# Kernel optimization log

Hardware: AMD Instinct MI355X
Metric: run time of the kernel (lower is better)

Reference implementation:

```python
import jax, jax.numpy as jnp
import numpy as np

N, B, D, K, H = 30000, 16, 32, 8, 8
DIST = 5.0
EPS = 1e-6


def setup_inputs() -> dict:
    key = jax.random.key(0)
    ks = jax.random.split(key, 16)
    sc = 1.0 / np.sqrt(D)
    inp = {
        'pos': jax.random.uniform(ks[0], (N, 3), jnp.float32) * 20.0,
        'node_features': jax.random.normal(ks[1], (N, D), jnp.float32),
        'batch': jnp.sort(jax.random.randint(ks[2], (N,), 0, B, dtype=jnp.int32)),
        'bessel_weights': jnp.linspace(jnp.pi, K * jnp.pi, K).astype(jnp.float32),
        'init_dummy': jax.random.normal(ks[3], (D,), jnp.float32),
        'Wq_dummy': jax.random.normal(ks[4], (D, D), jnp.float32) * sc,
        'Wq_graph': jax.random.normal(ks[5], (D, D), jnp.float32) * sc,
        'Wdot': jax.random.normal(ks[6], (D, D), jnp.float32) * sc,
        'W1_kd': jax.random.normal(ks[7], (K, H), jnp.float32) / np.sqrt(K),
        'W2_kd': jax.random.normal(ks[8], (H, D * D), jnp.float32) / np.sqrt(H),
        'W1_vd': jax.random.normal(ks[9], (K, H), jnp.float32) / np.sqrt(K),
        'W2_vd': jax.random.normal(ks[10], (H, D * D), jnp.float32) / np.sqrt(H),
        'W1_kg': jax.random.normal(ks[11], (K, H), jnp.float32) / np.sqrt(K),
        'W2_kg': jax.random.normal(ks[12], (H, D * D), jnp.float32) / np.sqrt(H),
        'W1_vg': jax.random.normal(ks[13], (K, H), jnp.float32) / np.sqrt(K),
        'W2_vg': jax.random.normal(ks[14], (H, D * D), jnp.float32) / np.sqrt(H),
    }
    return inp


def reference(pos, node_features, batch, bessel_weights, init_dummy,
              Wq_dummy, Wq_graph, Wdot,
              W1_kd, W2_kd, W1_vd, W2_vd, W1_kg, W2_kg, W1_vg, W2_vg):
    scale = 1.0 / np.sqrt(D)

    # --- dummy edge features: per-batch z extents + bessel basis ---
    z = pos[:, 2]                                            # [N]
    z_min = jax.ops.segment_min(z, batch, num_segments=B)    # [B]
    z_max = jax.ops.segment_max(z, batch, num_segments=B)    # [B]
    bot_len = z - z_min[batch] + DIST                        # [N]
    top_len = z_max[batch] + DIST - z                        # [N]

    def bessel(x):  # [N] -> [N,K]
        return jnp.sin(bessel_weights * x[:, None]) / (x[:, None] + EPS)

    edge = jnp.stack([bessel(bot_len), bessel(top_len)], axis=1)  # [N,2,K]

    # --- init dummy node features [B, 2, D] ---
    dummy = jnp.broadcast_to(init_dummy, (B, 2, D))

    def gen_w(W1, W2):  # conditional weight generator (silu MLP)
        return (jax.nn.silu(edge @ W1) @ W2).reshape(N, 2, D, D)

    # --- dummy nodes attend over graph nodes (segment softmax) ---
    wk = gen_w(W1_kd, W2_kd)                                 # [N,2,D,D]
    wv = gen_w(W1_vd, W2_vd)
    q = (dummy @ Wq_dummy)[batch]                            # [N,2,D]
    k = jnp.einsum('nd,nsde->nse', node_features, wk)        # [N,2,D]
    v = jnp.einsum('nd,nsde->nse', node_features, wv)
    s = jnp.einsum('nsq,qk,nsk->ns', q, Wdot, k) * scale     # [N,2]
    m = jax.ops.segment_max(s, batch, num_segments=B)
    e = jnp.exp(s - m[batch])
    zsum = jax.ops.segment_sum(e, batch, num_segments=B)
    attn = e / zsum[batch]                                   # [N,2]
    dummy_new = dummy + jax.ops.segment_sum(attn[..., None] * v, batch, num_segments=B)

    # --- graph nodes attend over (2) dummy nodes ---
    wkg = gen_w(W1_kg, W2_kg)
    wvg = gen_w(W1_vg, W2_vg)
    d_per = dummy_new[batch]                                 # [N,2,D]
    kg = jnp.einsum('nsd,nsde->nse', d_per, wkg)
    vg = jnp.einsum('nsd,nsde->nse', d_per, wvg)
    qg = node_features @ Wq_graph                            # [N,D]
    sg = jnp.einsum('nq,qk,nsk->ns', qg, Wdot, kg) * scale   # [N,2]
    ag = jax.nn.softmax(sg, axis=1)
    x_new = node_features + jnp.einsum('ns,nsd->nd', ag, vg)  # [N,D]
    return x_new
```

## Files before the change

kernel.cpp:

```cpp
#include <hip/hip_runtime.h>
#include <math.h>

#define NN 30000
#define BB 16
#define DD 32
#define KK 8
#define HH 8
#define DIST_C 5.0f
#define EPS_C 1e-6f
#define SCALE_C 0.17677669529663687f

#define WS_ZMIN 0
#define WS_ZMAX 16
#define WS_ZSUM 32
#define WS_QW   64
#define WS_PK   96
#define WS_WC   352
#define WS_T    1376
#define WS_AKG  9568
#define WS_AVG  17760

__device__ __forceinline__ unsigned fencode(float f) {
    unsigned u = __float_as_uint(f);
    return (u & 0x80000000u) ? ~u : (u | 0x80000000u);
}
__device__ __forceinline__ float fdecode(unsigned c) {
    return __uint_as_float((c & 0x80000000u) ? (c ^ 0x80000000u) : ~c);
}
__device__ __forceinline__ float silu(float x) { return x / (1.0f + expf(-x)); }

__global__ __launch_bounds__(256) void k_init(const float* __restrict__ init_dummy,
                                              const float* __restrict__ Wq_dummy,
                                              const float* __restrict__ Wdot,
                                              const float* __restrict__ W2_kd,
                                              const float* __restrict__ Wq_graph,
                                              float* __restrict__ ws) {
    __shared__ float qvec[32];
    __shared__ float qWl[32];
    int t = threadIdx.x;
    unsigned* wsu = (unsigned*)ws;
    if (t < 16) { wsu[WS_ZMIN + t] = 0xFFFFFFFFu; wsu[WS_ZMAX + t] = 0u; }
    if (t < 32) ws[WS_ZSUM + t] = 0.0f;
    for (int i = t; i < 8192; i += 256) ws[WS_T + i] = 0.0f;
    if (t < 32) {
        float acc = 0.0f;
        for (int d = 0; d < 32; ++d) acc += init_dummy[d] * Wq_dummy[d * 32 + t];
        qvec[t] = acc;
    }
    __syncthreads();
    if (t < 32) {
        float acc = 0.0f;
        for (int e = 0; e < 32; ++e) acc += qvec[e] * Wdot[e * 32 + t];
        qWl[t] = acc;
        ws[WS_QW + t] = acc;
    }
    __syncthreads();
    {
        int h = t >> 5, d = t & 31;
        float acc = 0.0f;
        for (int e = 0; e < 32; ++e) acc += W2_kd[h * 1024 + d * 32 + e] * qWl[e];
        ws[WS_PK + t] = acc;
    }
    for (int i = t; i < 1024; i += 256) {
        int d = i >> 5, e = i & 31;
        float acc = 0.0f;
        for (int m = 0; m < 32; ++m) acc += Wq_graph[d * 32 + m] * Wdot[m * 32 + e];
        ws[WS_WC + i] = acc;
    }
}

__global__ __launch_bounds__(256) void k_zminmax(const float* __restrict__ pos,
                                                 const int* __restrict__ batch,
                                                 float* __restrict__ ws) {
    __shared__ unsigned zl[16], zh[16];
    int t = threadIdx.x;
    if (t < 16) { zl[t] = 0xFFFFFFFFu; zh[t] = 0u; }
    __syncthreads();
    int n = blockIdx.x * 256 + t;
    if (n < NN) {
        unsigned c = fencode(pos[3 * n + 2]);
        int b = batch[n];
        atomicMin(&zl[b], c);
        atomicMax(&zh[b], c);
    }
    __syncthreads();
    unsigned* wsu = (unsigned*)ws;
    if (t < 16) {
        if (zl[t] != 0xFFFFFFFFu) atomicMin(&wsu[WS_ZMIN + t], zl[t]);
        if (zh[t] != 0u)          atomicMax(&wsu[WS_ZMAX + t], zh[t]);
    }
}

#define LWS 17
#define LFS 36
__global__ __launch_bounds__(256) void k_phase1(const float* __restrict__ pos,
                                                const int* __restrict__ batch,
                                                const float* __restrict__ nf,
                                                const float* __restrict__ bw,
                                                const float* __restrict__ W1_kd,
                                                const float* __restrict__ W1_vd,
                                                float* __restrict__ ws) {
    __shared__ float Lw[256 * LWS];
    __shared__ float Lf[256 * LFS];
    __shared__ int   Lb[256];
    __shared__ float W1kd[64], W1vd[64], Pk[256], zsl[32], bwl[8];
    int t = threadIdx.x;
    if (t < 64) { W1kd[t] = W1_kd[t]; W1vd[t] = W1_vd[t]; }
    Pk[t] = ws[WS_PK + t];
    if (t < 32) zsl[t] = 0.0f;
    if (t < 8) bwl[t] = bw[t];
    __syncthreads();

    int n = blockIdx.x * 256 + t;
    if (n < NN) {
        int b = batch[n];
        unsigned* wsu = (unsigned*)ws;
        float z = pos[3 * n + 2];
        float zmin = fdecode(wsu[WS_ZMIN + b]);
        float zmax = fdecode(wsu[WS_ZMAX + b]);
        float xl[2];
        xl[0] = z - zmin + DIST_C;
        xl[1] = zmax + DIST_C - z;
        float edge[2][8];
        #pragma unroll
        for (int s = 0; s < 2; ++s) {
            float inv = 1.0f / (xl[s] + EPS_C);
            #pragma unroll
            for (int k = 0; k < 8; ++k) edge[s][k] = sinf(bwl[k] * xl[s]) * inv;
        }
        float f[32];
        const float4* nf4 = (const float4*)nf;
        float4* Lf4 = (float4*)Lf;
        #pragma unroll
        for (int j = 0; j < 8; ++j) {
            float4 v = nf4[n * 8 + j];
            f[4 * j] = v.x; f[4 * j + 1] = v.y; f[4 * j + 2] = v.z; f[4 * j + 3] = v.w;
            Lf4[t * 9 + j] = v;
        }
        float u[8];
        #pragma unroll
        for (int h = 0; h < 8; ++h) {
            float acc = 0.0f;
            #pragma unroll
            for (int d = 0; d < 32; ++d) acc += f[d] * Pk[h * 32 + d];
            u[h] = acc;
        }
        float ev[2];
        #pragma unroll
        for (int s = 0; s < 2; ++s) {
            float sacc = 0.0f;
            #pragma unroll
            for (int h = 0; h < 8; ++h) {
                float pre = 0.0f;
                #pragma unroll
                for (int k = 0; k < 8; ++k) pre += edge[s][k] * W1kd[k * 8 + h];
                sacc += silu(pre) * u[h];
            }
            ev[s] = expf(sacc * SCALE_C);
            atomicAdd(&zsl[b * 2 + s], ev[s]);
        }
        #pragma unroll
        for (int s = 0; s < 2; ++s) {
            #pragma unroll
            for (int h = 0; h < 8; ++h) {
                float pre = 0.0f;
                #pragma unroll
                for (int k = 0; k < 8; ++k) pre += edge[s][k] * W1vd[k * 8 + h];
                Lw[t * LWS + s * 8 + h] = ev[s] * silu(pre);
            }
        }
        Lb[t] = b;
    } else {
        Lb[t] = -1;
    }
    __syncthreads();
    if (t < 32 && zsl[t] != 0.0f) atomicAdd(&ws[WS_ZSUM + t], zsl[t]);

    int base = blockIdx.x * 256;
    int count = NN - base; if (count > 256) count = 256;
    int bf = Lb[0], bl = Lb[count - 1];
    int wave = t >> 6, lane = t & 63;
    int sh = lane & 15;
    int dg = lane >> 4;
    int i0 = wave * 64;
    int i1 = i0 + 64; if (i1 > count) i1 = count;
    const float4* Lf4r = (const float4*)Lf;
    for (int b2 = bf; b2 <= bl; ++b2) {
        float a0 = 0.f, a1 = 0.f, a2 = 0.f, a3 = 0.f;
        float a4 = 0.f, a5 = 0.f, a6 = 0.f, a7 = 0.f;
        for (int i = i0; i < i1; ++i) {
            if (Lb[i] != b2) continue;
            float w = Lw[i * LWS + sh];
            float4 x0 = Lf4r[i * 9 + 2 * dg];
            float4 x1 = Lf4r[i * 9 + 2 * dg + 1];
            a0 += w * x0.x; a1 += w * x0.y; a2 += w * x0.z; a3 += w * x0.w;
            a4 += w * x1.x; a5 += w * x1.y; a6 += w * x1.z; a7 += w * x1.w;
        }
        float* Tb = ws + WS_T + b2 * 512 + sh * 32 + dg * 8;
        atomicAdd(&Tb[0], a0); atomicAdd(&Tb[1], a1);
        atomicAdd(&Tb[2], a2); atomicAdd(&Tb[3], a3);
        atomicAdd(&Tb[4], a4); atomicAdd(&Tb[5], a5);
        atomicAdd(&Tb[6], a6); atomicAdd(&Tb[7], a7);
    }
}

__global__ __launch_bounds__(256) void k_batch(const float* __restrict__ init_dummy,
                                               const float* __restrict__ W2_vd,
                                               const float* __restrict__ W2_kg,
                                               const float* __restrict__ W2_vg,
                                               float* __restrict__ ws) {
    int bs = blockIdx.x;
    int b = bs >> 1, s = bs & 1;
    int t = threadIdx.x;
    __shared__ float Tl[256];
    __shared__ float dn[32];
    Tl[t] = ws[WS_T + b * 512 + s * 256 + t];
    __syncthreads();
    if (t < 32) {
        float acc = 0.0f;
        #pragma unroll
        for (int h = 0; h < 8; ++h) {
            #pragma unroll
            for (int d = 0; d < 32; ++d)
                acc += Tl[h * 32 + d] * W2_vd[h * 1024 + d * 32 + t];
        }
        float zs = ws[WS_ZSUM + b * 2 + s];
        dn[t] = init_dummy[t] + acc / zs;
    }
    __syncthreads();
    {
        int h = t >> 5, e = t & 31;
        float ak = 0.0f, av = 0.0f;
        #pragma unroll
        for (int d = 0; d < 32; ++d) {
            float dv = dn[d];
            ak += dv * W2_kg[h * 1024 + d * 32 + e];
            av += dv * W2_vg[h * 1024 + d * 32 + e];
        }
        ws[WS_AKG + b * 512 + s * 256 + t] = ak;
        ws[WS_AVG + b * 512 + s * 256 + t] = av;
    }
}

__global__ __launch_bounds__(256) void k_final(const float* __restrict__ pos,
                                               const int* __restrict__ batch,
                                               const float* __restrict__ nf,
                                               const float* __restrict__ bw,
                                               const float* __restrict__ W1_kg,
                                               const float* __restrict__ W1_vg,
                                               const float* __restrict__ ws,
                                               float* __restrict__ out) {
    __shared__ float Wc[1024];
    __shared__ float W1kg[64], W1vg[64], bwl[8];
    int t = threadIdx.x;
    for (int i = t; i < 1024; i += 256) Wc[i] = ws[WS_WC + i];
    if (t < 64) { W1kg[t] = W1_kg[t]; W1vg[t] = W1_vg[t]; }
    if (t < 8) bwl[t] = bw[t];
    __syncthreads();
    int n = blockIdx.x * 256 + t;
    if (n >= NN) return;

    int b = batch[n];
    const unsigned* wsu = (const unsigned*)ws;
    float z = pos[3 * n + 2];
    float zmin = fdecode(wsu[WS_ZMIN + b]);
    float zmax = fdecode(wsu[WS_ZMAX + b]);
    float xl[2];
    xl[0] = z - zmin + DIST_C;
    xl[1] = zmax + DIST_C - z;
    float edge[2][8];
    #pragma unroll
    for (int s = 0; s < 2; ++s) {
        float inv = 1.0f / (xl[s] + EPS_C);
        #pragma unroll
        for (int k = 0; k < 8; ++k) edge[s][k] = sinf(bwl[k] * xl[s]) * inv;
    }
    float akg[2][8], avgg[2][8];
    #pragma unroll
    for (int s = 0; s < 2; ++s) {
        #pragma unroll
        for (int h = 0; h < 8; ++h) {
            float pk = 0.0f, pv = 0.0f;
            #pragma unroll
            for (int k = 0; k < 8; ++k) {
                pk += edge[s][k] * W1kg[k * 8 + h];
                pv += edge[s][k] * W1vg[k * 8 + h];
            }
            akg[s][h] = silu(pk);
            avgg[s][h] = silu(pv);
        }
    }
    float f[32];
    const float4* nf4 = (const float4*)nf;
    float4 fv4[8];
    #pragma unroll
    for (int j = 0; j < 8; ++j) {
        float4 v = nf4[n * 8 + j];
        fv4[j] = v;
        f[4 * j] = v.x; f[4 * j + 1] = v.y; f[4 * j + 2] = v.z; f[4 * j + 3] = v.w;
    }
    float4 q4[8];
    #pragma unroll
    for (int j = 0; j < 8; ++j) { q4[j].x = 0; q4[j].y = 0; q4[j].z = 0; q4[j].w = 0; }
    const float4* Wc4 = (const float4*)Wc;
    #pragma unroll
    for (int d = 0; d < 32; ++d) {
        float fd = f[d];
        #pragma unroll
        for (int j = 0; j < 8; ++j) {
            float4 w = Wc4[d * 8 + j];
            q4[j].x += fd * w.x; q4[j].y += fd * w.y; q4[j].z += fd * w.z; q4[j].w += fd * w.w;
        }
    }
    const float4* Ak4 = (const float4*)(ws + WS_AKG);
    const float4* Av4 = (const float4*)(ws + WS_AVG);
    float sg[2];
    #pragma unroll
    for (int s = 0; s < 2; ++s) {
        float acc = 0.0f;
        #pragma unroll
        for (int h = 0; h < 8; ++h) {
            int rb = b * 128 + s * 64 + h * 8;
            float dotv = 0.0f;
            #pragma unroll
            for (int j = 0; j < 8; ++j) {
                float4 a = Ak4[rb + j];
                dotv += q4[j].x * a.x + q4[j].y * a.y + q4[j].z * a.z + q4[j].w * a.w;
            }
            acc += akg[s][h] * dotv;
        }
        sg[s] = acc * SCALE_C;
    }
    float mm = fmaxf(sg[0], sg[1]);
    float e0 = expf(sg[0] - mm), e1 = expf(sg[1] - mm);
    float inv = 1.0f / (e0 + e1);
    float ag0 = e0 * inv, ag1 = e1 * inv;
    float4 x4[8];
    #pragma unroll
    for (int j = 0; j < 8; ++j) x4[j] = fv4[j];
    #pragma unroll
    for (int s = 0; s < 2; ++s) {
        float ags = (s == 0) ? ag0 : ag1;
        #pragma unroll
        for (int h = 0; h < 8; ++h) {
            float wv = ags * avgg[s][h];
            int rb = b * 128 + s * 64 + h * 8;
            #pragma unroll
            for (int j = 0; j < 8; ++j) {
                float4 a = Av4[rb + j];
                x4[j].x += wv * a.x; x4[j].y += wv * a.y; x4[j].z += wv * a.z; x4[j].w += wv * a.w;
            }
        }
    }
    float4* out4 = (float4*)out;
    #pragma unroll
    for (int j = 0; j < 8; ++j) out4[n * 8 + j] = x4[j];
}

extern "C" void kernel_launch(void* const* d_in, const int* in_sizes, int n_in,
                              void* d_out, int out_size, void* d_ws, size_t ws_size,
                              hipStream_t stream) {
    const float* pos        = (const float*)d_in[0];
    const float* nf         = (const float*)d_in[1];
    const int*   batch      = (const int*)d_in[2];
    const float* bw         = (const float*)d_in[3];
    const float* init_dummy = (const float*)d_in[4];
    const float* Wq_dummy   = (const float*)d_in[5];
    const float* Wq_graph   = (const float*)d_in[6];
    const float* Wdot       = (const float*)d_in[7];
    const float* W1_kd      = (const float*)d_in[8];
    const float* W2_kd      = (const float*)d_in[9];
    const float* W1_vd      = (const float*)d_in[10];
    const float* W2_vd      = (const float*)d_in[11];
    const float* W1_kg      = (const float*)d_in[12];
    const float* W2_kg      = (const float*)d_in[13];
    const float* W1_vg      = (const float*)d_in[14];
    const float* W2_vg      = (const float*)d_in[15];
    float* ws  = (float*)d_ws;
    float* out = (float*)d_out;

    int nblk = (NN + 255) / 256;
    hipLaunchKernelGGL(k_init, dim3(1), dim3(256), 0, stream,
                       init_dummy, Wq_dummy, Wdot, W2_kd, Wq_graph, ws);
    hipLaunchKernelGGL(k_zminmax, dim3(nblk), dim3(256), 0, stream, pos, batch, ws);
    hipLaunchKernelGGL(k_phase1, dim3(nblk), dim3(256), 0, stream,
                       pos, batch, nf, bw, W1_kd, W1_vd, ws);
    hipLaunchKernelGGL(k_batch, dim3(32), dim3(256), 0, stream,
                       init_dummy, W2_vd, W2_kg, W2_vg, ws);
    hipLaunchKernelGGL(k_final, dim3(nblk), dim3(256), 0, stream,
                       pos, batch, nf, bw, W1_kg, W1_vg, ws, out);
}
```

Baseline: 147.0 us.

## Fuse all stages into one persistent kernel with grid-wide atomic barriers

Replaces the five launches (init, z min/max, phase1, per-batch, final) with one 118-block kernel. Three spin-wait grid barriers on a workspace counter, cleared by a memset, separate the stages. Per-node data (features, edge basis, all four W1 projections, the query) stays in registers and is no longer recomputed or reloaded in the final stage. Z extents are reduced through per-block partials instead of global atomics. The cost is barrier spin overhead, more register pressure, and reliance on all blocks being co-resident, which 118 blocks on this GPU should satisfy.

```diff
diff --git a/kernel.cpp b/kernel.cpp
--- a/kernel.cpp
+++ b/kernel.cpp
@@ -3,22 +3,21 @@
 
 #define NN 30000
 #define BB 16
-#define DD 32
-#define KK 8
-#define HH 8
+#define NBLK 118
 #define DIST_C 5.0f
 #define EPS_C 1e-6f
 #define SCALE_C 0.17677669529663687f
 
-#define WS_ZMIN 0
-#define WS_ZMAX 16
-#define WS_ZSUM 32
-#define WS_QW   64
-#define WS_PK   96
-#define WS_WC   352
-#define WS_T    1376
-#define WS_AKG  9568
-#define WS_AVG  17760
+#define WS_BAR  0
+#define WS_PZM  8
+#define WS_PZX  2056
+#define WS_ZSUM 4104
+#define WS_T    4136
+#define WS_AKG  12328
+#define WS_AVG  20520
+
+#define LWS 17
+#define LFS 36
 
 __device__ __forceinline__ unsigned fencode(float f) {
     unsigned u = __float_as_uint(f);
@@ -29,95 +28,129 @@
 }
 __device__ __forceinline__ float silu(float x) { return x / (1.0f + expf(-x)); }
 
-__global__ __launch_bounds__(256) void k_init(const float* __restrict__ init_dummy,
-                                              const float* __restrict__ Wq_dummy,
-                                              const float* __restrict__ Wdot,
-                                              const float* __restrict__ W2_kd,
-                                              const float* __restrict__ Wq_graph,
-                                              float* __restrict__ ws) {
-    __shared__ float qvec[32];
-    __shared__ float qWl[32];
+__device__ __forceinline__ void gbarrier(unsigned* cnt, unsigned target) {
+    __syncthreads();
+    if (threadIdx.x == 0) {
+        __threadfence();
+        __hip_atomic_fetch_add(cnt, 1u, __ATOMIC_ACQ_REL, __HIP_MEMORY_SCOPE_AGENT);
+        while (__hip_atomic_load(cnt, __ATOMIC_ACQUIRE, __HIP_MEMORY_SCOPE_AGENT) < target) {
+            __builtin_amdgcn_s_sleep(2);
+        }
+    }
+    __syncthreads();
+}
+
+__global__ __launch_bounds__(256) void k_fused(
+    const float* __restrict__ pos, const int* __restrict__ batch,
+    const float* __restrict__ nf, const float* __restrict__ bw,
+    const float* __restrict__ init_dummy, const float* __restrict__ Wq_dummy,
+    const float* __restrict__ Wq_graph, const float* __restrict__ Wdot,
+    const float* __restrict__ W1_kd, const float* __restrict__ W2_kd,
+    const float* __restrict__ W1_vd, const float* __restrict__ W2_vd,
+    const float* __restrict__ W1_kg, const float* __restrict__ W2_kg,
+    const float* __restrict__ W1_vg, const float* __restrict__ W2_vg,
+    float* __restrict__ ws, float* __restrict__ out)
+{
+    __shared__ float Lw[256 * LWS];
+    __shared__ float Lf[256 * LFS];
+    __shared__ int   Lb[256];
+    __shared__ float W1kd[64], W1vd[64], W1kg[64], W1vg[64];
+    __shared__ float Pk[256], Wc[1024], qv[64], zsl[32], bwl[8];
+    __shared__ unsigned zl[16], zh[16];
+
     int t = threadIdx.x;
     unsigned* wsu = (unsigned*)ws;
-    if (t < 16) { wsu[WS_ZMIN + t] = 0xFFFFFFFFu; wsu[WS_ZMAX + t] = 0u; }
-    if (t < 32) ws[WS_ZSUM + t] = 0.0f;
-    for (int i = t; i < 8192; i += 256) ws[WS_T + i] = 0.0f;
+    unsigned* barc = wsu + WS_BAR;
+
+    if (t < 64) { W1kd[t] = W1_kd[t]; W1vd[t] = W1_vd[t];
+                  W1kg[t] = W1_kg[t]; W1vg[t] = W1_vg[t]; }
+    if (t < 8)  bwl[t] = bw[t];
+    if (t < 16) { zl[t] = 0u; zh[t] = 0u; }
+    if (t < 32) zsl[t] = 0.0f;
     if (t < 32) {
         float acc = 0.0f;
         for (int d = 0; d < 32; ++d) acc += init_dummy[d] * Wq_dummy[d * 32 + t];
-        qvec[t] = acc;
+        qv[t] = acc;
     }
     __syncthreads();
     if (t < 32) {
         float acc = 0.0f;
-        for (int e = 0; e < 32; ++e) acc += qvec[e] * Wdot[e * 32 + t];
-        qWl[t] = acc;
-        ws[WS_QW + t] = acc;
+        for (int e = 0; e < 32; ++e) acc += qv[e] * Wdot[e * 32 + t];
+        qv[32 + t] = acc;
+    }
+
+    int n = blockIdx.x * 256 + t;
+    bool act = n < NN;
+    float z = 0.0f; int b = 0;
+    float f[32]; float4 fv4[8];
+    #pragma unroll
+    for (int j = 0; j < 8; ++j) { fv4[j].x = fv4[j].y = fv4[j].z = fv4[j].w = 0.0f; }
+    if (act) {
+        z = pos[3 * n + 2];
+        b = batch[n];
+        const float4* nf4 = (const float4*)nf;
+        float4* Lf4 = (float4*)Lf;
+        #pragma unroll
+        for (int j = 0; j < 8; ++j) {
+            float4 v = nf4[n * 8 + j];
+            fv4[j] = v;
+            f[4*j] = v.x; f[4*j+1] = v.y; f[4*j+2] = v.z; f[4*j+3] = v.w;
+            Lf4[t * 9 + j] = v;
+        }
+        atomicMax(&zl[b], fencode(-z));
+        atomicMax(&zh[b], fencode(z));
+        Lb[t] = b;
+    } else {
+        #pragma unroll
+        for (int j = 0; j < 32; ++j) f[j] = 0.0f;
+        Lb[t] = -1;
     }
     __syncthreads();
     {
         int h = t >> 5, d = t & 31;
         float acc = 0.0f;
-        for (int e = 0; e < 32; ++e) acc += W2_kd[h * 1024 + d * 32 + e] * qWl[e];
-        ws[WS_PK + t] = acc;
+        for (int e = 0; e < 32; ++e) acc += W2_kd[h * 1024 + d * 32 + e] * qv[32 + e];
+        Pk[t] = acc;
     }
     for (int i = t; i < 1024; i += 256) {
         int d = i >> 5, e = i & 31;
         float acc = 0.0f;
         for (int m = 0; m < 32; ++m) acc += Wq_graph[d * 32 + m] * Wdot[m * 32 + e];
-        ws[WS_WC + i] = acc;
-    }
-}
-
-__global__ __launch_bounds__(256) void k_zminmax(const float* __restrict__ pos,
-                                                 const int* __restrict__ batch,
-                                                 float* __restrict__ ws) {
-    __shared__ unsigned zl[16], zh[16];
-    int t = threadIdx.x;
-    if (t < 16) { zl[t] = 0xFFFFFFFFu; zh[t] = 0u; }
-    __syncthreads();
-    int n = blockIdx.x * 256 + t;
-    if (n < NN) {
-        unsigned c = fencode(pos[3 * n + 2]);
-        int b = batch[n];
-        atomicMin(&zl[b], c);
-        atomicMax(&zh[b], c);
-    }
-    __syncthreads();
-    unsigned* wsu = (unsigned*)ws;
+        Wc[i] = acc;
+    }
     if (t < 16) {
-        if (zl[t] != 0xFFFFFFFFu) atomicMin(&wsu[WS_ZMIN + t], zl[t]);
-        if (zh[t] != 0u)          atomicMax(&wsu[WS_ZMAX + t], zh[t]);
-    }
-}
-
-#define LWS 17
-#define LFS 36
-__global__ __launch_bounds__(256) void k_phase1(const float* __restrict__ pos,
-                                                const int* __restrict__ batch,
-                                                const float* __restrict__ nf,
-                                                const float* __restrict__ bw,
-                                                const float* __restrict__ W1_kd,
-                                                const float* __restrict__ W1_vd,
-                                                float* __restrict__ ws) {
-    __shared__ float Lw[256 * LWS];
-    __shared__ float Lf[256 * LFS];
-    __shared__ int   Lb[256];
-    __shared__ float W1kd[64], W1vd[64], Pk[256], zsl[32], bwl[8];
-    int t = threadIdx.x;
-    if (t < 64) { W1kd[t] = W1_kd[t]; W1vd[t] = W1_vd[t]; }
-    Pk[t] = ws[WS_PK + t];
-    if (t < 32) zsl[t] = 0.0f;
-    if (t < 8) bwl[t] = bw[t];
-    __syncthreads();
-
-    int n = blockIdx.x * 256 + t;
-    if (n < NN) {
-        int b = batch[n];
-        unsigned* wsu = (unsigned*)ws;
-        float z = pos[3 * n + 2];
-        float zmin = fdecode(wsu[WS_ZMIN + b]);
-        float zmax = fdecode(wsu[WS_ZMAX + b]);
+        wsu[WS_PZM + t * 128 + blockIdx.x] = zl[t];
+        wsu[WS_PZX + t * 128 + blockIdx.x] = zh[t];
+        zl[t] = 0u; zh[t] = 0u;
+    }
+    {
+        int g = blockIdx.x * 256 + t;
+        if (g < 8224) ws[WS_ZSUM + g] = 0.0f;
+    }
+    gbarrier(barc, NBLK);
+
+    {
+        int b4 = t >> 4, c = t & 15;
+        unsigned m0 = 0u, m1 = 0u;
+        int i0 = c * 8, i1 = i0 + 8; if (i1 > NBLK) i1 = NBLK;
+        for (int i = i0; i < i1; ++i) {
+            unsigned p0 = wsu[WS_PZM + b4 * 128 + i];
+            unsigned p1 = wsu[WS_PZX + b4 * 128 + i];
+            m0 = m0 > p0 ? m0 : p0;
+            m1 = m1 > p1 ? m1 : p1;
+        }
+        atomicMax(&zl[b4], m0);
+        atomicMax(&zh[b4], m1);
+    }
+    __syncthreads();
+
+    float akg[2][8], avgg[2][8];
+    float4 q4[8];
+    #pragma unroll
+    for (int j = 0; j < 8; ++j) { q4[j].x = q4[j].y = q4[j].z = q4[j].w = 0.0f; }
+    {
+        float zmin = -fdecode(zl[b]);
+        float zmax =  fdecode(zh[b]);
         float xl[2];
         xl[0] = z - zmin + DIST_C;
         xl[1] = zmax + DIST_C - z;
@@ -128,15 +161,6 @@
             #pragma unroll
             for (int k = 0; k < 8; ++k) edge[s][k] = sinf(bwl[k] * xl[s]) * inv;
         }
-        float f[32];
-        const float4* nf4 = (const float4*)nf;
-        float4* Lf4 = (float4*)Lf;
-        #pragma unroll
-        for (int j = 0; j < 8; ++j) {
-            float4 v = nf4[n * 8 + j];
-            f[4 * j] = v.x; f[4 * j + 1] = v.y; f[4 * j + 2] = v.z; f[4 * j + 3] = v.w;
-            Lf4[t * 9 + j] = v;
-        }
         float u[8];
         #pragma unroll
         for (int h = 0; h < 8; ++h) {
@@ -145,216 +169,152 @@
             for (int d = 0; d < 32; ++d) acc += f[d] * Pk[h * 32 + d];
             u[h] = acc;
         }
-        float ev[2];
         #pragma unroll
         for (int s = 0; s < 2; ++s) {
             float sacc = 0.0f;
             #pragma unroll
             for (int h = 0; h < 8; ++h) {
-                float pre = 0.0f;
+                float pkd = 0.0f, pvd = 0.0f, pkg = 0.0f, pvg = 0.0f;
                 #pragma unroll
-                for (int k = 0; k < 8; ++k) pre += edge[s][k] * W1kd[k * 8 + h];
-                sacc += silu(pre) * u[h];
-            }
-            ev[s] = expf(sacc * SCALE_C);
-            atomicAdd(&zsl[b * 2 + s], ev[s]);
-        }
+                for (int k = 0; k < 8; ++k) {
+                    float e8 = edge[s][k];
+                    pkd += e8 * W1kd[k * 8 + h];
+                    pvd += e8 * W1vd[k * 8 + h];
+                    pkg += e8 * W1kg[k * 8 + h];
+                    pvg += e8 * W1vg[k * 8 + h];
+                }
+                sacc += silu(pkd) * u[h];
+                Lw[t * LWS + s * 8 + h] = silu(pvd);
+                akg[s][h] = silu(pkg);
+                avgg[s][h] = silu(pvg);
+            }
+            float ev = act ? expf(sacc * SCALE_C) : 0.0f;
+            if (act) atomicAdd(&zsl[b * 2 + s], ev);
+            #pragma unroll
+            for (int h = 0; h < 8; ++h) Lw[t * LWS + s * 8 + h] *= ev;
+        }
+        const float4* Wc4 = (const float4*)Wc;
+        #pragma unroll
+        for (int d = 0; d < 32; ++d) {
+            float fd = f[d];
+            #pragma unroll
+            for (int j = 0; j < 8; ++j) {
+                float4 w = Wc4[d * 8 + j];
+                q4[j].x += fd * w.x; q4[j].y += fd * w.y;
+                q4[j].z += fd * w.z; q4[j].w += fd * w.w;
+            }
+        }
+    }
+    __syncthreads();
+    if (t < 32 && zsl[t] != 0.0f) atomicAdd(&ws[WS_ZSUM + t], zsl[t]);
+
+    {
+        int base = blockIdx.x * 256;
+        int count = NN - base; if (count > 256) count = 256;
+        int bf = Lb[0], bl = Lb[count - 1];
+        int wave = t >> 6, lane = t & 63;
+        int sh = lane & 15;
+        int dg = lane >> 4;
+        int i0 = wave * 64;
+        int i1 = i0 + 64; if (i1 > count) i1 = count;
+        const float4* Lf4r = (const float4*)Lf;
+        for (int b2 = bf; b2 <= bl; ++b2) {
+            float a0=0.f,a1=0.f,a2=0.f,a3=0.f,a4=0.f,a5=0.f,a6=0.f,a7=0.f;
+            for (int i = i0; i < i1; ++i) {
+                if (Lb[i] != b2) continue;
+                float w = Lw[i * LWS + sh];
+                float4 x0 = Lf4r[i * 9 + 2 * dg];
+                float4 x1 = Lf4r[i * 9 + 2 * dg + 1];
+                a0 += w * x0.x; a1 += w * x0.y; a2 += w * x0.z; a3 += w * x0.w;
+                a4 += w * x1.x; a5 += w * x1.y; a6 += w * x1.z; a7 += w * x1.w;
+            }
+            float* Tb = ws + WS_T + b2 * 512 + sh * 32 + dg * 8;
+            atomicAdd(&Tb[0], a0); atomicAdd(&Tb[1], a1);
+            atomicAdd(&Tb[2], a2); atomicAdd(&Tb[3], a3);
+            atomicAdd(&Tb[4], a4); atomicAdd(&Tb[5], a5);
+            atomicAdd(&Tb[6], a6); atomicAdd(&Tb[7], a7);
+        }
+    }
+    gbarrier(barc, 2 * NBLK);
+
+    if (blockIdx.x < 32) {
+        int b3 = blockIdx.x >> 1, s3 = blockIdx.x & 1;
+        float* Tl = Lf;
+        float* dn = Lf + 320;
+        Tl[t] = ws[WS_T + b3 * 512 + s3 * 256 + t];
+        __syncthreads();
+        if (t < 32) {
+            float acc = 0.0f;
+            #pragma unroll
+            for (int h = 0; h < 8; ++h)
+                #pragma unroll
+                for (int d = 0; d < 32; ++d)
+                    acc += Tl[h * 32 + d] * W2_vd[h * 1024 + d * 32 + t];
+            float zs = ws[WS_ZSUM + b3 * 2 + s3];
+            dn[t] = init_dummy[t] + acc / zs;
+        }
+        __syncthreads();
+        {
+            int h = t >> 5, e = t & 31;
+            float ak = 0.0f, av = 0.0f;
+            #pragma unroll
+            for (int d = 0; d < 32; ++d) {
+                float dv = dn[d];
+                ak += dv * W2_kg[h * 1024 + d * 32 + e];
+                av += dv * W2_vg[h * 1024 + d * 32 + e];
+            }
+            ws[WS_AKG + b3 * 512 + s3 * 256 + t] = ak;
+            ws[WS_AVG + b3 * 512 + s3 * 256 + t] = av;
+        }
+    }
+    gbarrier(barc, 3 * NBLK);
+
+    if (act) {
+        const float4* Ak4 = (const float4*)(ws + WS_AKG);
+        const float4* Av4 = (const float4*)(ws + WS_AVG);
+        float sg[2];
         #pragma unroll
         for (int s = 0; s < 2; ++s) {
+            float acc = 0.0f;
             #pragma unroll
             for (int h = 0; h < 8; ++h) {
-                float pre = 0.0f;
+                int rb = b * 128 + s * 64 + h * 8;
+                float dotv = 0.0f;
                 #pragma unroll
-                for (int k = 0; k < 8; ++k) pre += edge[s][k] * W1vd[k * 8 + h];
-                Lw[t * LWS + s * 8 + h] = ev[s] * silu(pre);
-            }
-        }
-        Lb[t] = b;
-    } else {
-        Lb[t] = -1;
-    }
-    __syncthreads();
-    if (t < 32 && zsl[t] != 0.0f) atomicAdd(&ws[WS_ZSUM + t], zsl[t]);
-
-    int base = blockIdx.x * 256;
-    int count = NN - base; if (count > 256) count = 256;
-    int bf = Lb[0], bl = Lb[count - 1];
-    int wave = t >> 6, lane = t & 63;
-    int sh = lane & 15;
-    int dg = lane >> 4;
-    int i0 = wave * 64;
-    int i1 = i0 + 64; if (i1 > count) i1 = count;
-    const float4* Lf4r = (const float4*)Lf;
-    for (int b2 = bf; b2 <= bl; ++b2) {
-        float a0 = 0.f, a1 = 0.f, a2 = 0.f, a3 = 0.f;
-        float a4 = 0.f, a5 = 0.f, a6 = 0.f, a7 = 0.f;
-        for (int i = i0; i < i1; ++i) {
-            if (Lb[i] != b2) continue;
-            float w = Lw[i * LWS + sh];
-            float4 x0 = Lf4r[i * 9 + 2 * dg];
-            float4 x1 = Lf4r[i * 9 + 2 * dg + 1];
-            a0 += w * x0.x; a1 += w * x0.y; a2 += w * x0.z; a3 += w * x0.w;
-            a4 += w * x1.x; a5 += w * x1.y; a6 += w * x1.z; a7 += w * x1.w;
-        }
-        float* Tb = ws + WS_T + b2 * 512 + sh * 32 + dg * 8;
-        atomicAdd(&Tb[0], a0); atomicAdd(&Tb[1], a1);
-        atomicAdd(&Tb[2], a2); atomicAdd(&Tb[3], a3);
-        atomicAdd(&Tb[4], a4); atomicAdd(&Tb[5], a5);
-        atomicAdd(&Tb[6], a6); atomicAdd(&Tb[7], a7);
-    }
-}
-
-__global__ __launch_bounds__(256) void k_batch(const float* __restrict__ init_dummy,
-                                               const float* __restrict__ W2_vd,
-                                               const float* __restrict__ W2_kg,
-                                               const float* __restrict__ W2_vg,
-                                               float* __restrict__ ws) {
-    int bs = blockIdx.x;
-    int b = bs >> 1, s = bs & 1;
-    int t = threadIdx.x;
-    __shared__ float Tl[256];
-    __shared__ float dn[32];
-    Tl[t] = ws[WS_T + b * 512 + s * 256 + t];
-    __syncthreads();
-    if (t < 32) {
-        float acc = 0.0f;
-        #pragma unroll
-        for (int h = 0; h < 8; ++h) {
-            #pragma unroll
-            for (int d = 0; d < 32; ++d)
-                acc += Tl[h * 32 + d] * W2_vd[h * 1024 + d * 32 + t];
-        }
-        float zs = ws[WS_ZSUM + b * 2 + s];
-        dn[t] = init_dummy[t] + acc / zs;
-    }
-    __syncthreads();
-    {
-        int h = t >> 5, e = t & 31;
-        float ak = 0.0f, av = 0.0f;
-        #pragma unroll
-        for (int d = 0; d < 32; ++d) {
-            float dv = dn[d];
-            ak += dv * W2_kg[h * 1024 + d * 32 + e];
-            av += dv * W2_vg[h * 1024 + d * 32 + e];
-        }
-        ws[WS_AKG + b * 512 + s * 256 + t] = ak;
-        ws[WS_AVG + b * 512 + s * 256 + t] = av;
-    }
-}
-
-__global__ __launch_bounds__(256) void k_final(const float* __restrict__ pos,
-                                               const int* __restrict__ batch,
-                                               const float* __restrict__ nf,
-                                               const float* __restrict__ bw,
-                                               const float* __restrict__ W1_kg,
-                                               const float* __restrict__ W1_vg,
-                                               const float* __restrict__ ws,
-                                               float* __restrict__ out) {
-    __shared__ float Wc[1024];
-    __shared__ float W1kg[64], W1vg[64], bwl[8];
-    int t = threadIdx.x;
-    for (int i = t; i < 1024; i += 256) Wc[i] = ws[WS_WC + i];
-    if (t < 64) { W1kg[t] = W1_kg[t]; W1vg[t] = W1_vg[t]; }
-    if (t < 8) bwl[t] = bw[t];
-    __syncthreads();
-    int n = blockIdx.x * 256 + t;
-    if (n >= NN) return;
-
-    int b = batch[n];
-    const unsigned* wsu = (const unsigned*)ws;
-    float z = pos[3 * n + 2];
-    float zmin = fdecode(wsu[WS_ZMIN + b]);
-    float zmax = fdecode(wsu[WS_ZMAX + b]);
-    float xl[2];
-    xl[0] = z - zmin + DIST_C;
-    xl[1] = zmax + DIST_C - z;
-    float edge[2][8];
-    #pragma unroll
-    for (int s = 0; s < 2; ++s) {
-        float inv = 1.0f / (xl[s] + EPS_C);
-        #pragma unroll
-        for (int k = 0; k < 8; ++k) edge[s][k] = sinf(bwl[k] * xl[s]) * inv;
-    }
-    float akg[2][8], avgg[2][8];
-    #pragma unroll
-    for (int s = 0; s < 2; ++s) {
-        #pragma unroll
-        for (int h = 0; h < 8; ++h) {
-            float pk = 0.0f, pv = 0.0f;
-            #pragma unroll
-            for (int k = 0; k < 8; ++k) {
-                pk += edge[s][k] * W1kg[k * 8 + h];
-                pv += edge[s][k] * W1vg[k * 8 + h];
-            }
-            akg[s][h] = silu(pk);
-            avgg[s][h] = silu(pv);
-        }
-    }
-    float f[32];
-    const float4* nf4 = (const float4*)nf;
-    float4 fv4[8];
-    #pragma unroll
-    for (int j = 0; j < 8; ++j) {
-        float4 v = nf4[n * 8 + j];
-        fv4[j] = v;
-        f[4 * j] = v.x; f[4 * j + 1] = v.y; f[4 * j + 2] = v.z; f[4 * j + 3] = v.w;
-    }
-    float4 q4[8];
-    #pragma unroll
-    for (int j = 0; j < 8; ++j) { q4[j].x = 0; q4[j].y = 0; q4[j].z = 0; q4[j].w = 0; }
-    const float4* Wc4 = (const float4*)Wc;
-    #pragma unroll
-    for (int d = 0; d < 32; ++d) {
-        float fd = f[d];
-        #pragma unroll
-        for (int j = 0; j < 8; ++j) {
-            float4 w = Wc4[d * 8 + j];
-            q4[j].x += fd * w.x; q4[j].y += fd * w.y; q4[j].z += fd * w.z; q4[j].w += fd * w.w;
-        }
-    }
-    const float4* Ak4 = (const float4*)(ws + WS_AKG);
-    const float4* Av4 = (const float4*)(ws + WS_AVG);
-    float sg[2];
-    #pragma unroll
-    for (int s = 0; s < 2; ++s) {
-        float acc = 0.0f;
-        #pragma unroll
-        for (int h = 0; h < 8; ++h) {
-            int rb = b * 128 + s * 64 + h * 8;
-            float dotv = 0.0f;
-            #pragma unroll
-            for (int j = 0; j < 8; ++j) {
-                float4 a = Ak4[rb + j];
-                dotv += q4[j].x * a.x + q4[j].y * a.y + q4[j].z * a.z + q4[j].w * a.w;
-            }
-            acc += akg[s][h] * dotv;
-        }
-        sg[s] = acc * SCALE_C;
-    }
-    float mm = fmaxf(sg[0], sg[1]);
-    float e0 = expf(sg[0] - mm), e1 = expf(sg[1] - mm);
-    float inv = 1.0f / (e0 + e1);
-    float ag0 = e0 * inv, ag1 = e1 * inv;
-    float4 x4[8];
-    #pragma unroll
-    for (int j = 0; j < 8; ++j) x4[j] = fv4[j];
-    #pragma unroll
-    for (int s = 0; s < 2; ++s) {
-        float ags = (s == 0) ? ag0 : ag1;
-        #pragma unroll
-        for (int h = 0; h < 8; ++h) {
-            float wv = ags * avgg[s][h];
-            int rb = b * 128 + s * 64 + h * 8;
-            #pragma unroll
-            for (int j = 0; j < 8; ++j) {
-                float4 a = Av4[rb + j];
-                x4[j].x += wv * a.x; x4[j].y += wv * a.y; x4[j].z += wv * a.z; x4[j].w += wv * a.w;
-            }
-        }
-    }
-    float4* out4 = (float4*)out;
-    #pragma unroll
-    for (int j = 0; j < 8; ++j) out4[n * 8 + j] = x4[j];
+                for (int j = 0; j < 8; ++j) {
+                    float4 a = Ak4[rb + j];
+                    dotv += q4[j].x * a.x + q4[j].y * a.y + q4[j].z * a.z + q4[j].w * a.w;
+                }
+                acc += akg[s][h] * dotv;
+            }
+            sg[s] = acc * SCALE_C;
+        }
+        float mm = fmaxf(sg[0], sg[1]);
+        float e0 = expf(sg[0] - mm), e1 = expf(sg[1] - mm);
+        float inv = 1.0f / (e0 + e1);
+        float ag0 = e0 * inv, ag1 = e1 * inv;
+        float4 x4[8];
+        #pragma unroll
+        for (int j = 0; j < 8; ++j) x4[j] = fv4[j];
+        #pragma unroll
+        for (int s = 0; s < 2; ++s) {
+            float ags = (s == 0) ? ag0 : ag1;
+            #pragma unroll
+            for (int h = 0; h < 8; ++h) {
+                float wv = ags * avgg[s][h];
+                int rb = b * 128 + s * 64 + h * 8;
+                #pragma unroll
+                for (int j = 0; j < 8; ++j) {
+                    float4 a = Av4[rb + j];
+                    x4[j].x += wv * a.x; x4[j].y += wv * a.y;
+                    x4[j].z += wv * a.z; x4[j].w += wv * a.w;
+                }
+            }
+        }
+        float4* out4 = (float4*)out;
+        #pragma unroll
+        for (int j = 0; j < 8; ++j) out4[n * 8 + j] = x4[j];
+    }
 }
 
 extern "C" void kernel_launch(void* const* d_in, const int* in_sizes, int n_in,
@@ -379,14 +339,10 @@
     float* ws  = (float*)d_ws;
     float* out = (float*)d_out;
 
-    int nblk = (NN + 255) / 256;
-    hipLaunchKernelGGL(k_init, dim3(1), dim3(256), 0, stream,
-                       init_dummy, Wq_dummy, Wdot, W2_kd, Wq_graph, ws);
-    hipLaunchKernelGGL(k_zminmax, dim3(nblk), dim3(256), 0, stream, pos, batch, ws);
-    hipLaunchKernelGGL(k_phase1, dim3(nblk), dim3(256), 0, stream,
-                       pos, batch, nf, bw, W1_kd, W1_vd, ws);
-    hipLaunchKernelGGL(k_batch, dim3(32), dim3(256), 0, stream,
-                       init_dummy, W2_vd, W2_kg, W2_vg, ws);
-    hipLaunchKernelGGL(k_final, dim3(nblk), dim3(256), 0, stream,
-                       pos, batch, nf, bw, W1_kg, W1_vg, ws, out);
-}
+    hipMemsetAsync(d_ws, 0x00, 32, stream);
+
+    hipLaunchKernelGGL(k_fused, dim3(NBLK), dim3(256), 0, stream,
+                       pos, batch, nf, bw, init_dummy, Wq_dummy, Wq_graph,
+                       Wdot, W1_kd, W2_kd, W1_vd, W2_vd, W1_kg, W2_kg,
+                       W1_vg, W2_vg, ws, out);
+}
```

Measured after the change: 420.8 us. +186.3%, slower.
